# Kernel tuning notes

Hardware: AMD Instinct MI355X
Metric: run time of the kernel (lower is better)

The kernel has to match this reference:

```python
import jax, jax.numpy as jnp
import numpy as np

B, N, C = 8, 1374, 768
H = 12
HD = C // H  # 64
HIDDEN = int(C * 4.0)  # 3072
EPS = 1e-5


def setup_inputs() -> dict:
    key = jax.random.key(0)
    ks = jax.random.split(key, 12)
    s = 0.02
    return {
        "x": jax.random.normal(ks[0], (B, N, C), jnp.float32),
        "rope_freqs": jax.random.normal(ks[1], (1, N, 1, HD), jnp.float32),
        "ln1_g": jnp.ones((C,), jnp.float32),
        "ln1_b": jnp.zeros((C,), jnp.float32),
        "qkv_w": jax.random.normal(ks[2], (3 * C, C), jnp.float32) * s,
        "qkv_b": jnp.zeros((3 * C,), jnp.float32),
        "proj_w": jax.random.normal(ks[3], (C, C), jnp.float32) * s,
        "proj_b": jnp.zeros((C,), jnp.float32),
        "ln2_g": jnp.ones((C,), jnp.float32),
        "ln2_b": jnp.zeros((C,), jnp.float32),
        "w1": jax.random.normal(ks[4], (HIDDEN, C), jnp.float32) * s,
        "b1": jnp.zeros((HIDDEN,), jnp.float32),
        "w2": jax.random.normal(ks[5], (HIDDEN, C), jnp.float32) * s,
        "b2": jnp.zeros((HIDDEN,), jnp.float32),
        "w3": jax.random.normal(ks[6], (C, HIDDEN), jnp.float32) * s,
        "b3": jnp.zeros((C,), jnp.float32),
    }


def _layernorm(x, g, b):
    mu = jnp.mean(x, axis=-1, keepdims=True)
    var = jnp.mean(jnp.square(x - mu), axis=-1, keepdims=True)
    return (x - mu) * jax.lax.rsqrt(var + EPS) * g + b


def _rotate_half(x):
    x1, x2 = jnp.split(x, 2, axis=-1)
    return jnp.concatenate([-x2, x1], axis=-1)


def _apply_rope(q, k, freqs):
    # freqs: [1, N, 1, HD] -> [1, 1, N, HD] (matches torch permute(0,2,1,3))
    f = jnp.transpose(freqs, (0, 2, 1, 3))
    cos, sin = jnp.cos(f), jnp.sin(f)
    q_rot = q * cos + _rotate_half(q) * sin
    k_rot = k * cos + _rotate_half(k) * sin
    return q_rot, k_rot


def reference(x, rope_freqs, ln1_g, ln1_b, qkv_w, qkv_b, proj_w, proj_b,
              ln2_g, ln2_b, w1, b1, w2, b2, w3, b3):
    scale = HD ** -0.5
    # --- Attention branch ---
    h = _layernorm(x, ln1_g, ln1_b)
    qkv = jnp.einsum('bnc,dc->bnd', h, qkv_w) + qkv_b          # [B,N,3C]
    qkv = qkv.reshape(B, N, 3, H, HD).transpose(2, 0, 3, 1, 4)  # [3,B,H,N,HD]
    q, k, v = qkv[0], qkv[1], qkv[2]
    # rope_freqs covers all N tokens -> n_special = 0 path
    q, k = _apply_rope(q, k, rope_freqs)
    attn = jnp.einsum('bhnd,bhmd->bhnm', q, k) * scale          # [B,H,N,N]
    attn = jax.nn.softmax(attn, axis=-1)
    o = jnp.einsum('bhnm,bhmd->bhnd', attn, v)                  # [B,H,N,HD]
    o = o.transpose(0, 2, 1, 3).reshape(B, N, C)
    o = jnp.einsum('bnc,dc->bnd', o, proj_w) + proj_b
    x = x + o
    # --- SwiGLU MLP branch ---
    h2 = _layernorm(x, ln2_g, ln2_b)
    x1 = jnp.einsum('bnc,hc->bnh', h2, w1) + b1
    x2 = jnp.einsum('bnc,hc->bnh', h2, w2) + b2
    hid = jax.nn.silu(x1) * x2
    mlp_out = jnp.einsum('bnh,ch->bnc', hid, w3) + b3
    return x + mlp_out
```

## Files before the change

kernel.cpp:

```cpp
#include <hip/hip_runtime.h>
#include <stdint.h>

#define B_ 8
#define N_ 1374
#define C_ 768
#define H_ 12
#define HD_ 64
#define HID_ 3072
#define M_ (B_*N_)
#define MPAD_ 11008
#define QT_ 22
#define QT2_ 11

typedef __attribute__((ext_vector_type(8))) short short8;
typedef __attribute__((ext_vector_type(4))) float f32x4;
typedef __attribute__((ext_vector_type(4))) _Float16 half4;

__device__ __forceinline__ unsigned short f2bf(float f) {
  unsigned u = __float_as_uint(f);
  u += 0x7FFF + ((u >> 16) & 1);
  return (unsigned short)(u >> 16);
}
__device__ __forceinline__ float bf2f(unsigned short h) {
  return __uint_as_float(((unsigned)h) << 16);
}

#if __has_builtin(__builtin_amdgcn_global_load_lds)
#define HAVE_GLL 1
#endif

__device__ __forceinline__ void gld16(const unsigned short* g, unsigned short* l) {
#ifdef HAVE_GLL
  __builtin_amdgcn_global_load_lds((const __attribute__((address_space(1))) void*)g,
                                   (__attribute__((address_space(3))) void*)l, 16, 0, 0);
#else
  *(short8*)l = *(const short8*)g;
#endif
}

__global__ __launch_bounds__(256) void cvt5_kernel(
    const float* __restrict__ s0, const float* __restrict__ s1,
    const float* __restrict__ s2, const float* __restrict__ s3,
    const float* __restrict__ s4, unsigned short* __restrict__ out) {
  int id = blockIdx.x * 256 + threadIdx.x;
  const float* src; int off;
  if (id < 442368)        { src = s0; off = id; }
  else if (id < 589824)   { src = s1; off = id - 442368; }
  else if (id < 1179648)  { src = s2; off = id - 589824; }
  else if (id < 1769472)  { src = s3; off = id - 1179648; }
  else                    { src = s4; off = id - 1769472; }
  float4 v = ((const float4*)src)[off];
  ushort4 o;
  o.x = f2bf(v.x); o.y = f2bf(v.y); o.z = f2bf(v.z); o.w = f2bf(v.w);
  ((ushort4*)out)[id] = o;
}

__global__ __launch_bounds__(256) void ln_kernel(const float* __restrict__ in,
    const float* __restrict__ g, const float* __restrict__ bta,
    unsigned short* __restrict__ out) {
  int row = blockIdx.x;
  int t = threadIdx.x;
  const float* xr = in + (size_t)row * C_;
  float v0 = xr[t], v1 = xr[t + 256], v2 = xr[t + 512];
  float s1 = v0 + v1 + v2;
  float s2 = v0*v0 + v1*v1 + v2*v2;
  for (int off = 1; off < 64; off <<= 1) {
    s1 += __shfl_xor(s1, off, 64);
    s2 += __shfl_xor(s2, off, 64);
  }
  __shared__ float r1[4], r2[4];
  int wave = t >> 6, lane = t & 63;
  if (lane == 0) { r1[wave] = s1; r2[wave] = s2; }
  __syncthreads();
  float tot1 = r1[0] + r1[1] + r1[2] + r1[3];
  float tot2 = r2[0] + r2[1] + r2[2] + r2[3];
  float mu = tot1 * (1.0f / C_);
  float var = tot2 * (1.0f / C_) - mu * mu;
  float rs = rsqrtf(var + 1e-5f);
  size_t ob = (size_t)row * C_;
  out[ob + t]       = f2bf((v0 - mu) * rs * g[t]       + bta[t]);
  out[ob + t + 256] = f2bf((v1 - mu) * rs * g[t + 256] + bta[t + 256]);
  out[ob + t + 512] = f2bf((v2 - mu) * rs * g[t + 512] + bta[t + 512]);
}

template<int EPI, int ROPE, int TM, int SWZ>
__global__ __launch_bounds__(256, (TM == 64) ? 4 : 2) void gemm_bt(
    const unsigned short* __restrict__ A,
    const unsigned short* __restrict__ W,
    void* __restrict__ outp,
    const float* __restrict__ bias0,
    const float* __restrict__ resid,
    const float* __restrict__ freqs,
    int K, int ldo, int Mvalid, int X)
{
  constexpr int MI = TM / 32;
  __shared__ __align__(16) unsigned short As[2][TM * 32];
  __shared__ __align__(16) unsigned short Bs[2][4096];
  const int t = threadIdx.x;
  const int lane = t & 63;
  const int wave = t >> 6;
  const int wm = (wave >> 1) * (TM / 2);
  const int wn = (wave & 1) * 64;
  const int lr = lane & 15;
  const int lg = lane >> 4;
  const int lk = lg * 8;
  int bx, by;
  if (SWZ) {
    int Y = gridDim.x / X;
    int lin = blockIdx.x;
    int sgsz = X * 8;
    int sg = lin / sgsz;
    int base_y = sg * 8;
    int rows = Y - base_y; if (rows > 8) rows = 8;
    int within = lin - sg * sgsz;
    by = base_y + within % rows;
    bx = within / rows;
  } else {
    bx = blockIdx.x % X;
    by = blockIdx.x / X;
  }
  const int tm0 = by * TM;
  const int tn0 = bx * 128;
  const int r0 = t >> 2;
  const int c0 = (t & 3) * 8;
  const unsigned short* ga0 = A + (size_t)(tm0 + r0) * K + c0;
  const unsigned short* ga1 = A + (size_t)(tm0 + 64 + r0) * K + c0;
  const unsigned short* gb0 = W + (size_t)(tn0 + r0) * K + c0;
  const unsigned short* gb1 = W + (size_t)(tn0 + 64 + r0) * K + c0;
  f32x4 zero = {0.f, 0.f, 0.f, 0.f};
  f32x4 acc[MI][4];
#pragma unroll
  for (int mi = 0; mi < MI; ++mi)
#pragma unroll
    for (int ni = 0; ni < 4; ++ni) acc[mi][ni] = zero;

  for (int kt = 0; kt < K; kt += 64) {
    __syncthreads();
    gld16(ga0 + kt,      &As[0][t * 8]);
    gld16(ga0 + kt + 32, &As[1][t * 8]);
    if (TM == 128) {
      gld16(ga1 + kt,      &As[0][2048 + t * 8]);
      gld16(ga1 + kt + 32, &As[1][2048 + t * 8]);
    }
    gld16(gb0 + kt,      &Bs[0][t * 8]);
    gld16(gb1 + kt,      &Bs[0][2048 + t * 8]);
    gld16(gb0 + kt + 32, &Bs[1][t * 8]);
    gld16(gb1 + kt + 32, &Bs[1][2048 + t * 8]);
    __syncthreads();
#pragma unroll
    for (int u = 0; u < 2; ++u) {
      short8 af[MI], bfr[4];
#pragma unroll
      for (int mi = 0; mi < MI; ++mi) af[mi] = *(const short8*)&As[u][(wm + mi * 16 + lr) * 32 + lk];
#pragma unroll
      for (int ni = 0; ni < 4; ++ni) bfr[ni] = *(const short8*)&Bs[u][(wn + ni * 16 + lr) * 32 + lk];
#pragma unroll
      for (int mi = 0; mi < MI; ++mi)
#pragma unroll
        for (int ni = 0; ni < 4; ++ni)
          acc[mi][ni] = __builtin_amdgcn_mfma_f32_16x16x32_bf16(af[mi], bfr[ni], acc[mi][ni], 0, 0, 0);
    }
  }

  if (EPI == 0) {
    bool dorope = ROPE && ((tn0 + wn) < 1536);
#pragma unroll
    for (int mi = 0; mi < MI; ++mi) {
#pragma unroll
      for (int p = 0; p < 2; ++p) {
        int col1 = tn0 + wn + p * 16 + lr;
        int col2 = col1 + 32;
        float bv1 = bias0[col1], bv2 = bias0[col2];
        int e = p * 16 + lr;
#pragma unroll
        for (int r = 0; r < 4; ++r) {
          int row = tm0 + wm + mi * 16 + lg * 4 + r;
          float v1 = acc[mi][p][r] + bv1;
          float v2 = acc[mi][p + 2][r] + bv2;
          float o1 = v1, o2 = v2;
          if (dorope) {
            int n = row % N_;
            float f1 = freqs[n * HD_ + e];
            float f2 = freqs[n * HD_ + e + 32];
            float c1, s1, c2, s2;
            __sincosf(f1, &s1, &c1);
            __sincosf(f2, &s2, &c2);
            o1 = v1 * c1 - v2 * s1;
            o2 = v2 * c2 + v1 * s2;
          }
          size_t base = (size_t)row * ldo;
          ((unsigned short*)outp)[base + col1] = f2bf(o1);
          ((unsigned short*)outp)[base + col2] = f2bf(o2);
        }
      }
    }
  } else {
#pragma unroll
    for (int mi = 0; mi < MI; ++mi) {
#pragma unroll
      for (int ni = 0; ni < 4; ++ni) {
        int col = tn0 + wn + ni * 16 + lr;
        float bval = bias0[col];
#pragma unroll
        for (int r = 0; r < 4; ++r) {
          int row = tm0 + wm + mi * 16 + lg * 4 + r;
          float v = acc[mi][ni][r] + bval;
          size_t idx = (size_t)row * ldo + col;
          if (EPI == 1) {
            if (row < Mvalid) ((float*)outp)[idx] = resid[idx] + v;
          } else {
            if (row < Mvalid) ((float*)outp)[idx] = ((float*)outp)[idx] + v;
          }
        }
      }
    }
  }
}

__global__ __launch_bounds__(256, 2) void gemm_w12_swiglu(
    const unsigned short* __restrict__ A,
    const unsigned short* __restrict__ W1,
    const unsigned short* __restrict__ W2,
    unsigned short* __restrict__ hid,
    const float* __restrict__ b1,
    const float* __restrict__ b2)
{
  __shared__ __align__(16) unsigned short As[2][4096];
  __shared__ __align__(16) unsigned short B1s[2][2048];
  __shared__ __align__(16) unsigned short B2s[2][2048];
  const int t = threadIdx.x;
  const int lane = t & 63;
  const int wave = t >> 6;
  const int wm = (wave >> 1) * 64;
  const int wn = (wave & 1) * 32;
  const int lr = lane & 15;
  const int lg = lane >> 4;
  const int lk = lg * 8;
  const int tm0 = blockIdx.y * 128;
  const int tn0 = blockIdx.x * 64;
  const int r0 = t >> 2;
  const int c0 = (t & 3) * 8;
  const unsigned short* ga0 = A + (size_t)(tm0 + r0) * 768 + c0;
  const unsigned short* ga1 = A + (size_t)(tm0 + 64 + r0) * 768 + c0;
  const unsigned short* g1 = W1 + (size_t)(tn0 + r0) * 768 + c0;
  const unsigned short* g2 = W2 + (size_t)(tn0 + r0) * 768 + c0;
  f32x4 zero = {0.f, 0.f, 0.f, 0.f};
  f32x4 acc1[4][2], acc2[4][2];
#pragma unroll
  for (int mi = 0; mi < 4; ++mi)
#pragma unroll
    for (int ni = 0; ni < 2; ++ni) { acc1[mi][ni] = zero; acc2[mi][ni] = zero; }

  for (int kt = 0; kt < 768; kt += 64) {
    __syncthreads();
    gld16(ga0 + kt,      &As[0][t * 8]);
    gld16(ga1 + kt,      &As[0][2048 + t * 8]);
    gld16(ga0 + kt + 32, &As[1][t * 8]);
    gld16(ga1 + kt + 32, &As[1][2048 + t * 8]);
    gld16(g1 + kt,       &B1s[0][t * 8]);
    gld16(g1 + kt + 32,  &B1s[1][t * 8]);
    gld16(g2 + kt,       &B2s[0][t * 8]);
    gld16(g2 + kt + 32,  &B2s[1][t * 8]);
    __syncthreads();
#pragma unroll
    for (int u = 0; u < 2; ++u) {
      short8 af[4], b1f[2], b2f[2];
#pragma unroll
      for (int mi = 0; mi < 4; ++mi) af[mi] = *(const short8*)&As[u][(wm + mi * 16 + lr) * 32 + lk];
#pragma unroll
      for (int ni = 0; ni < 2; ++ni) {
        b1f[ni] = *(const short8*)&B1s[u][(wn + ni * 16 + lr) * 32 + lk];
        b2f[ni] = *(const short8*)&B2s[u][(wn + ni * 16 + lr) * 32 + lk];
      }
#pragma unroll
      for (int mi = 0; mi < 4; ++mi)
#pragma unroll
        for (int ni = 0; ni < 2; ++ni) {
          acc1[mi][ni] = __builtin_amdgcn_mfma_f32_16x16x32_bf16(af[mi], b1f[ni], acc1[mi][ni], 0, 0, 0);
          acc2[mi][ni] = __builtin_amdgcn_mfma_f32_16x16x32_bf16(af[mi], b2f[ni], acc2[mi][ni], 0, 0, 0);
        }
    }
  }
#pragma unroll
  for (int mi = 0; mi < 4; ++mi) {
#pragma unroll
    for (int ni = 0; ni < 2; ++ni) {
      int col = tn0 + wn + ni * 16 + lr;
      float bv1 = b1[col], bv2 = b2[col];
#pragma unroll
      for (int r = 0; r < 4; ++r) {
        int row = tm0 + wm + mi * 16 + lg * 4 + r;
        float a1 = acc1[mi][ni][r] + bv1;
        float a2 = acc2[mi][ni][r] + bv2;
        float h = a1 / (1.f + __expf(-a1)) * a2;
        hid[(size_t)row * HID_ + col] = f2bf(h);
      }
    }
  }
}

__global__ __launch_bounds__(256, 2) void attn_kernel(
    const unsigned short* __restrict__ qkv,
    unsigned short* __restrict__ o2)
{
  __shared__ __align__(16) unsigned short Ks[64 * 80];
  __shared__ __align__(16) _Float16 Vt[64 * 72];
  int bidx = blockIdx.x;
  int qt = bidx % QT2_;
  int bh = bidx / QT2_;
  int head = bh % H_;
  int b = bh / H_;
  int t = threadIdx.x, lane = t & 63, wave = t >> 6;
  int lr = lane & 15, lg = lane >> 4;

  short8 bq[2][2];
#pragma unroll
  for (int s = 0; s < 2; ++s) {
    int m = qt * 128 + wave * 32 + s * 16 + lr;
    int mc = (m < N_) ? m : (N_ - 1);
    const unsigned short* qrow = qkv + (size_t)(b * N_ + mc) * 2304 + head * HD_;
    bq[s][0] = *(const short8*)(qrow + lg * 8);
    bq[s][1] = *(const short8*)(qrow + 32 + lg * 8);
  }

  f32x4 zero = {0.f, 0.f, 0.f, 0.f};
  f32x4 acc[2][4];
#pragma unroll
  for (int s = 0; s < 2; ++s)
#pragma unroll
    for (int dt = 0; dt < 4; ++dt) acc[s][dt] = zero;
  float den[2] = {0.f, 0.f};

  const int vp = t & 31;
  const int vc = t >> 5;

  for (int jt = 0; jt < QT_; ++jt) {
    __syncthreads();
#pragma unroll
    for (int u = t; u < 512; u += 256) {
      int row = u >> 3, c = u & 7;
      int j = jt * 64 + row;
      int jc = (j < N_) ? j : (N_ - 1);
      const unsigned short* src = qkv + (size_t)(b * N_ + jc) * 2304 + 768 + head * HD_ + c * 8;
      *(short8*)&Ks[row * 80 + c * 8] = *(const short8*)src;
    }
    {
      int j0 = jt * 64 + 2 * vp;
      int j1 = j0 + 1;
      int j0c = (j0 < N_) ? j0 : (N_ - 1);
      int j1c = (j1 < N_) ? j1 : (N_ - 1);
      const unsigned short* s0 = qkv + (size_t)(b * N_ + j0c) * 2304 + 1536 + head * HD_ + vc * 8;
      const unsigned short* s1 = qkv + (size_t)(b * N_ + j1c) * 2304 + 1536 + head * HD_ + vc * 8;
      short8 v0 = *(const short8*)s0;
      short8 v1 = *(const short8*)s1;
#pragma unroll
      for (int i = 0; i < 8; ++i) {
        _Float16 lo = (_Float16)bf2f((unsigned short)v0[i]);
        _Float16 hi = (_Float16)bf2f((unsigned short)v1[i]);
        unsigned w = (unsigned)__builtin_bit_cast(unsigned short, lo)
                   | ((unsigned)__builtin_bit_cast(unsigned short, hi) << 16);
        *(unsigned*)&Vt[(vc * 8 + i) * 72 + 2 * vp] = w;
      }
    }
    __syncthreads();
#pragma unroll
    for (int st = 0; st < 4; ++st) {
      short8 ak0 = *(const short8*)&Ks[(st * 16 + lr) * 80 + lg * 8];
      short8 ak1 = *(const short8*)&Ks[(st * 16 + lr) * 80 + 32 + lg * 8];
      int jb = jt * 64 + st * 16 + lg * 4;
      half4 pf[2];
#pragma unroll
      for (int s = 0; s < 2; ++s) {
        f32x4 sc = zero;
        sc = __builtin_amdgcn_mfma_f32_16x16x32_bf16(ak0, bq[s][0], sc, 0, 0, 0);
        sc = __builtin_amdgcn_mfma_f32_16x16x32_bf16(ak1, bq[s][1], sc, 0, 0, 0);
        float dsum = 0.f;
#pragma unroll
        for (int r = 0; r < 4; ++r) {
          float pv = (jb + r < N_) ? __expf(sc[r] * 0.125f) : 0.f;
          dsum += pv;
          pf[s][r] = (_Float16)pv;
        }
        den[s] += dsum;
      }
#pragma unroll
      for (int dt = 0; dt < 4; ++dt) {
        half4 bv = *(const half4*)&Vt[(dt * 16 + lr) * 72 + st * 16 + lg * 4];
        acc[0][dt] = __builtin_amdgcn_mfma_f32_16x16x16f16(pf[0], bv, acc[0][dt], 0, 0, 0);
        acc[1][dt] = __builtin_amdgcn_mfma_f32_16x16x16f16(pf[1], bv, acc[1][dt], 0, 0, 0);
      }
    }
  }
#pragma unroll
  for (int s = 0; s < 2; ++s) {
    den[s] += __shfl_xor(den[s], 16, 64);
    den[s] += __shfl_xor(den[s], 32, 64);
  }
#pragma unroll
  for (int s = 0; s < 2; ++s) {
#pragma unroll
    for (int r = 0; r < 4; ++r) {
      float dm = __shfl(den[s], lg * 4 + r, 64);
      int m = qt * 128 + wave * 32 + s * 16 + lg * 4 + r;
      if (m < N_) {
        float invd = 1.f / dm;
        unsigned short* orow = o2 + (size_t)(b * N_ + m) * C_ + head * HD_;
#pragma unroll
        for (int dt = 0; dt < 4; ++dt)
          orow[dt * 16 + lr] = f2bf(acc[s][dt][r] * invd);
      }
    }
  }
}

extern "C" void kernel_launch(void* const* d_in, const int* in_sizes, int n_in,
                              void* d_out, int out_size, void* d_ws, size_t ws_size,
                              hipStream_t stream) {
  const float* x      = (const float*)d_in[0];
  const float* freqs  = (const float*)d_in[1];
  const float* ln1_g  = (const float*)d_in[2];
  const float* ln1_b  = (const float*)d_in[3];
  const float* qkv_w  = (const float*)d_in[4];
  const float* qkv_b  = (const float*)d_in[5];
  const float* proj_w = (const float*)d_in[6];
  const float* proj_b = (const float*)d_in[7];
  const float* ln2_g  = (const float*)d_in[8];
  const float* ln2_b  = (const float*)d_in[9];
  const float* w1     = (const float*)d_in[10];
  const float* b1     = (const float*)d_in[11];
  const float* w2     = (const float*)d_in[12];
  const float* b2     = (const float*)d_in[13];
  const float* w3     = (const float*)d_in[14];
  const float* b3     = (const float*)d_in[15];
  float* out = (float*)d_out;
  char* ws = (char*)d_ws;

  unsigned short* hB     = (unsigned short*)(ws + 0);
  unsigned short* wqkvB  = (unsigned short*)(ws + 16908288);
  unsigned short* wprojB = (unsigned short*)(ws + 20447232);
  unsigned short* w12B   = (unsigned short*)(ws + 21626880);
  unsigned short* w3B    = (unsigned short*)(ws + 31064064);
  unsigned short* qkvB   = (unsigned short*)(ws + 35782656);
  unsigned short* o2B    = (unsigned short*)(ws + 86507520);
  unsigned short* hidB   = qkvB;

  cvt5_kernel<<<9216, 256, 0, stream>>>(qkv_w, proj_w, w1, w2, w3, wqkvB);

  ln_kernel<<<M_, 256, 0, stream>>>(x, ln1_g, ln1_b, hB);
  gemm_bt<0, 1, 128, 1><<<18 * 86, 256, 0, stream>>>(hB, wqkvB, qkvB, qkv_b, nullptr, freqs, 768, 2304, M_, 18);
  attn_kernel<<<B_ * H_ * QT2_, 256, 0, stream>>>(qkvB, o2B);
  gemm_bt<1, 0, 64, 1><<<6 * 172, 256, 0, stream>>>(o2B, wprojB, out, proj_b, x, nullptr, 768, 768, M_, 6);

  ln_kernel<<<M_, 256, 0, stream>>>(out, ln2_g, ln2_b, hB);
  gemm_w12_swiglu<<<dim3(48, 86), 256, 0, stream>>>(hB, w12B, w12B + 3072 * 768, hidB, b1, b2);
  gemm_bt<3, 0, 64, 1><<<6 * 172, 256, 0, stream>>>(hidB, w3B, out, b3, nullptr, nullptr, 3072, 768, M_, 6);
}
```

Before: 543.3 us.

## Double-buffer attention K/V tiles with register prefetch and cheaper softmax exp

The attention kernel now keeps two LDS buffers for K and transposed V. It prefetches the next tile's K/V into registers while computing the current tile, which removes one __syncthreads per iteration and hides global load latency. The exponent uses exp2f with a prescaled constant, and the fp16 conversions use packed round-toward-zero. The key-bound mask now applies only on the last tile. The cost is double the LDS, more registers, and slightly different rounding in the P and V conversions. Issue(QT_) on the last iteration does a redundant clamped load.

```diff
diff --git a/kernel.cpp b/kernel.cpp
--- a/kernel.cpp
+++ b/kernel.cpp
@@ -15,6 +15,7 @@
 typedef __attribute__((ext_vector_type(8))) short short8;
 typedef __attribute__((ext_vector_type(4))) float f32x4;
 typedef __attribute__((ext_vector_type(4))) _Float16 half4;
+typedef __attribute__((ext_vector_type(2))) _Float16 half2v;
 
 __device__ __forceinline__ unsigned short f2bf(float f) {
   unsigned u = __float_as_uint(f);
@@ -23,6 +24,10 @@
 }
 __device__ __forceinline__ float bf2f(unsigned short h) {
   return __uint_as_float(((unsigned)h) << 16);
+}
+
+__device__ __forceinline__ half2v pkrtz(float a, float b) {
+  return __builtin_bit_cast(half2v, __builtin_amdgcn_cvt_pkrtz(a, b));
 }
 
 #if __has_builtin(__builtin_amdgcn_global_load_lds)
@@ -299,12 +304,15 @@
   }
 }
 
+struct FalseT { static constexpr bool value = false; };
+struct TrueT  { static constexpr bool value = true;  };
+
 __global__ __launch_bounds__(256, 2) void attn_kernel(
     const unsigned short* __restrict__ qkv,
     unsigned short* __restrict__ o2)
 {
-  __shared__ __align__(16) unsigned short Ks[64 * 80];
-  __shared__ __align__(16) _Float16 Vt[64 * 72];
+  __shared__ __align__(16) unsigned short Ks[2][64 * 80];
+  __shared__ __align__(16) _Float16 Vt[2][64 * 72];
   int bidx = blockIdx.x;
   int qt = bidx % QT2_;
   int bh = bidx / QT2_;
@@ -331,42 +339,31 @@
     for (int dt = 0; dt < 4; ++dt) acc[s][dt] = zero;
   float den[2] = {0.f, 0.f};
 
-  const int vp = t & 31;
-  const int vc = t >> 5;
-
-  for (int jt = 0; jt < QT_; ++jt) {
-    __syncthreads();
-#pragma unroll
-    for (int u = t; u < 512; u += 256) {
-      int row = u >> 3, c = u & 7;
-      int j = jt * 64 + row;
-      int jc = (j < N_) ? j : (N_ - 1);
-      const unsigned short* src = qkv + (size_t)(b * N_ + jc) * 2304 + 768 + head * HD_ + c * 8;
-      *(short8*)&Ks[row * 80 + c * 8] = *(const short8*)src;
-    }
-    {
-      int j0 = jt * 64 + 2 * vp;
-      int j1 = j0 + 1;
-      int j0c = (j0 < N_) ? j0 : (N_ - 1);
-      int j1c = (j1 < N_) ? j1 : (N_ - 1);
-      const unsigned short* s0 = qkv + (size_t)(b * N_ + j0c) * 2304 + 1536 + head * HD_ + vc * 8;
-      const unsigned short* s1 = qkv + (size_t)(b * N_ + j1c) * 2304 + 1536 + head * HD_ + vc * 8;
-      short8 v0 = *(const short8*)s0;
-      short8 v1 = *(const short8*)s1;
-#pragma unroll
-      for (int i = 0; i < 8; ++i) {
-        _Float16 lo = (_Float16)bf2f((unsigned short)v0[i]);
-        _Float16 hi = (_Float16)bf2f((unsigned short)v1[i]);
-        unsigned w = (unsigned)__builtin_bit_cast(unsigned short, lo)
-                   | ((unsigned)__builtin_bit_cast(unsigned short, hi) << 16);
-        *(unsigned*)&Vt[(vc * 8 + i) * 72 + 2 * vp] = w;
-      }
-    }
-    __syncthreads();
+  const int kr0 = t >> 3;
+  const int kc  = (t & 7) * 8;
+  const int vp  = t & 31;
+  const int vc  = t >> 5;
+  const unsigned short* kbase = qkv + (size_t)(b * N_) * 2304 + 768  + head * HD_ + kc;
+  const unsigned short* vbase = qkv + (size_t)(b * N_) * 2304 + 1536 + head * HD_ + vc * 8;
+
+  short8 krg[2], vrg[2];
+  auto issue = [&](int jt) {
+    int j0 = jt * 64 + kr0;        if (j0 >= N_) j0 = N_ - 1;
+    int j1 = jt * 64 + kr0 + 32;   if (j1 >= N_) j1 = N_ - 1;
+    int vj0 = jt * 64 + 2 * vp;    if (vj0 >= N_) vj0 = N_ - 1;
+    int vj1 = jt * 64 + 2 * vp + 1; if (vj1 >= N_) vj1 = N_ - 1;
+    krg[0] = *(const short8*)(kbase + (size_t)j0 * 2304);
+    krg[1] = *(const short8*)(kbase + (size_t)j1 * 2304);
+    vrg[0] = *(const short8*)(vbase + (size_t)vj0 * 2304);
+    vrg[1] = *(const short8*)(vbase + (size_t)vj1 * 2304);
+  };
+
+  auto compute = [&](int jt, const unsigned short* ksb, const _Float16* vtb, auto tailc) {
+    constexpr bool TAIL = decltype(tailc)::value;
 #pragma unroll
     for (int st = 0; st < 4; ++st) {
-      short8 ak0 = *(const short8*)&Ks[(st * 16 + lr) * 80 + lg * 8];
-      short8 ak1 = *(const short8*)&Ks[(st * 16 + lr) * 80 + 32 + lg * 8];
+      short8 ak0 = *(const short8*)&ksb[(st * 16 + lr) * 80 + lg * 8];
+      short8 ak1 = *(const short8*)&ksb[(st * 16 + lr) * 80 + 32 + lg * 8];
       int jb = jt * 64 + st * 16 + lg * 4;
       half4 pf[2];
 #pragma unroll
@@ -374,23 +371,49 @@
         f32x4 sc = zero;
         sc = __builtin_amdgcn_mfma_f32_16x16x32_bf16(ak0, bq[s][0], sc, 0, 0, 0);
         sc = __builtin_amdgcn_mfma_f32_16x16x32_bf16(ak1, bq[s][1], sc, 0, 0, 0);
-        float dsum = 0.f;
+        float p[4];
 #pragma unroll
         for (int r = 0; r < 4; ++r) {
-          float pv = (jb + r < N_) ? __expf(sc[r] * 0.125f) : 0.f;
-          dsum += pv;
-          pf[s][r] = (_Float16)pv;
+          float pv = exp2f(sc[r] * 0.18033688011112f);
+          if (TAIL) pv = (jb + r < N_) ? pv : 0.f;
+          p[r] = pv;
         }
-        den[s] += dsum;
+        den[s] += (p[0] + p[1]) + (p[2] + p[3]);
+        union { half4 v; half2v h[2]; } pu;
+        pu.h[0] = pkrtz(p[0], p[1]);
+        pu.h[1] = pkrtz(p[2], p[3]);
+        pf[s] = pu.v;
       }
 #pragma unroll
       for (int dt = 0; dt < 4; ++dt) {
-        half4 bv = *(const half4*)&Vt[(dt * 16 + lr) * 72 + st * 16 + lg * 4];
+        half4 bv = *(const half4*)&vtb[(dt * 16 + lr) * 72 + st * 16 + lg * 4];
         acc[0][dt] = __builtin_amdgcn_mfma_f32_16x16x16f16(pf[0], bv, acc[0][dt], 0, 0, 0);
         acc[1][dt] = __builtin_amdgcn_mfma_f32_16x16x16f16(pf[1], bv, acc[1][dt], 0, 0, 0);
       }
     }
-  }
+  };
+
+  issue(0);
+  int cur = 0;
+  for (int jt = 0; jt < QT_; ++jt) {
+    unsigned short* ksb = &Ks[cur][0];
+    _Float16* vtb = &Vt[cur][0];
+    *(short8*)&ksb[kr0 * 80 + kc] = krg[0];
+    *(short8*)&ksb[(kr0 + 32) * 80 + kc] = krg[1];
+#pragma unroll
+    for (int i = 0; i < 8; ++i) {
+      float lo = bf2f((unsigned short)vrg[0][i]);
+      float hi = bf2f((unsigned short)vrg[1][i]);
+      half2v w = pkrtz(lo, hi);
+      *(half2v*)&vtb[(vc * 8 + i) * 72 + 2 * vp] = w;
+    }
+    __syncthreads();
+    issue(jt + 1);
+    if (jt == QT_ - 1) compute(jt, ksb, vtb, TrueT{});
+    else               compute(jt, ksb, vtb, FalseT{});
+    cur ^= 1;
+  }
+
 #pragma unroll
   for (int s = 0; s < 2; ++s) {
     den[s] += __shfl_xor(den[s], 16, 64);
```

Measured after the change: 551.9 us. Within noise of the previous version (+1.6%).
